# Kernel tuning notes

Measured on AMD Instinct MI355X. Metric: run time of the kernel, lower is better.

## Reference

```python
import jax, jax.numpy as jnp
import numpy as np

C = 1.0                      # curvature
PHI = 3.1415926 * 0.3        # Cosine phase (bias=False path)
ALPHA = 0.2                  # LeakyReLU negative slope
A_PARA = 0.5                 # a_para_GATLayer
EPS = 4e-3                   # float32 ball-projection epsilon (standard HGCN)
MIN_NORM = 1e-15
NEG_INF = -9e15              # matches -9000000000000000.0 in source


def project(x, c):
    # clamp points to lie inside the Poincare ball of curvature c
    norm = jnp.maximum(jnp.linalg.norm(x, axis=-1, keepdims=True), MIN_NORM)
    maxnorm = (1.0 - EPS) / jnp.sqrt(c)
    return jnp.where(norm > maxnorm, x / norm * maxnorm, x)


def artanh(x):
    return jnp.arctanh(jnp.clip(x, -1.0 + 1e-7, 1.0 - 1e-7))


def logmap0(p, c):
    # log map at the origin of the Poincare ball
    sqrt_c = c ** 0.5
    p_norm = jnp.maximum(jnp.linalg.norm(p, axis=-1, keepdims=True), MIN_NORM)
    return artanh(sqrt_c * p_norm) / (sqrt_c * p_norm) * p


def setup_inputs() -> dict:
    key = jax.random.key(0)
    k1, k2, k3, k4 = jax.random.split(key, 4)
    N, FIN, FOUT = 8192, 512, 128
    h = jax.random.normal(k1, (N, FIN), dtype=jnp.float32)
    adj = jax.random.randint(k2, (N, N), 0, 2, dtype=jnp.int32)
    # xavier_uniform with gain=1.414
    lim_w = 1.414 * np.sqrt(6.0 / (FIN + FOUT))
    W = jax.random.uniform(k3, (FIN, FOUT), jnp.float32, -lim_w, lim_w)
    lim_a = 1.414 * np.sqrt(6.0 / (2 * FOUT + 1))
    a = jax.random.uniform(k4, (2 * FOUT, 1), jnp.float32, -lim_a, lim_a)
    return {"h": h, "adj": adj, "W": W, "a": a}


def reference(h, adj, W, a):
    fout = W.shape[1]
    Wh = h @ W                                   # [N, F_out]
    Wh1 = Wh @ a[:fout]                          # [N, 1] source score
    Wh2 = Wh @ a[fout:]                          # [N, 1] target score
    e = jax.nn.leaky_relu(Wh1 + Wh2.T, ALPHA)    # [N, N]
    e = jnp.where(adj > 0, e, NEG_INF)
    attention = jax.nn.softmax(e, axis=1)        # dropout p=0 (eval): identity
    h_prime = attention @ Wh                     # [N, F_out]
    h_prime = logmap0(project(h_prime, C), C)
    # concat=True branch: ELU + a_para * A*cos(x + phi), A=1 (data_dim=-1)
    return jax.nn.elu(h_prime) + A_PARA * jnp.cos(h_prime + PHI)
```

## Files before the change

### kernel.cpp

```cpp
#include <hip/hip_runtime.h>
#include <hip/hip_bf16.h>
#include <math.h>

typedef short short8 __attribute__((ext_vector_type(8)));
typedef float f32x4 __attribute__((ext_vector_type(4)));

static constexpr int N = 8192;
static constexpr int FIN = 512;
static constexpr int FOUT = 128;
static constexpr float PHI = 3.1415926f * 0.3f;
static constexpr float A_PARA = 0.5f;
static constexpr float EPS_BALL = 4e-3f;
static constexpr float L2E = 1.4426950408889634f;

__device__ __forceinline__ unsigned short f2b(float f) {
    union { float f; unsigned u; } v; v.f = f;
    unsigned r = v.u + 0x7fffu + ((v.u >> 16) & 1u);
    return (unsigned short)(r >> 16);
}

__device__ __forceinline__ unsigned f2key(float x) {
    unsigned b = __float_as_uint(x);
    return (b & 0x80000000u) ? ~b : (b | 0x80000000u);
}
__device__ __forceinline__ float key2f(unsigned k) {
    unsigned b = (k & 0x80000000u) ? (k ^ 0x80000000u) : ~k;
    return __uint_as_float(b);
}

__device__ __forceinline__ short8 cvt8(float4 x0, float4 x1) {
    short8 r;
    r[0] = (short)f2b(x0.x); r[1] = (short)f2b(x0.y);
    r[2] = (short)f2b(x0.z); r[3] = (short)f2b(x0.w);
    r[4] = (short)f2b(x1.x); r[5] = (short)f2b(x1.y);
    r[6] = (short)f2b(x1.z); r[7] = (short)f2b(x1.w);
    return r;
}

__device__ __forceinline__ void cw(float* w, const int4 a, const float4 tv,
                                   float sA, float mA) {
    float z;
    z = sA + tv.x; w[0] = a.x > 0 ? __builtin_amdgcn_exp2f(fmaxf(z, 0.2f * z) - mA) : 0.f;
    z = sA + tv.y; w[1] = a.y > 0 ? __builtin_amdgcn_exp2f(fmaxf(z, 0.2f * z) - mA) : 0.f;
    z = sA + tv.z; w[2] = a.z > 0 ? __builtin_amdgcn_exp2f(fmaxf(z, 0.2f * z) - mA) : 0.f;
    z = sA + tv.w; w[3] = a.w > 0 ? __builtin_amdgcn_exp2f(fmaxf(z, 0.2f * z) - mA) : 0.f;
}

__global__ __launch_bounds__(256) void k0_wt(const float* __restrict__ W,
                                             unsigned short* __restrict__ Wt,
                                             unsigned* __restrict__ Tkey,
                                             float* __restrict__ denb) {
    __shared__ float sh[32][33];
    const int t = threadIdx.x;
    const int k0 = (blockIdx.x >> 2) * 32, c0 = (blockIdx.x & 3) * 32;
    {
        int r = t >> 3, c4 = (t & 7) * 4;
        float4 v = *(const float4*)(W + (size_t)(k0 + r) * FOUT + c0 + c4);
        sh[r][c4] = v.x; sh[r][c4 + 1] = v.y; sh[r][c4 + 2] = v.z; sh[r][c4 + 3] = v.w;
    }
    __syncthreads();
    int cc = t >> 3, k4 = (t & 7) * 4;
    ushort4 o;
    o.x = f2b(sh[k4][cc]); o.y = f2b(sh[k4 + 1][cc]);
    o.z = f2b(sh[k4 + 2][cc]); o.w = f2b(sh[k4 + 3][cc]);
    *(ushort4*)(Wt + (size_t)(c0 + cc) * FIN + k0 + k4) = o;
    if (blockIdx.x == 0) {
        if (t == 0) Tkey[0] = 0u;
        for (int i = t; i < N; i += 256) denb[i] = 0.f;
    }
}

__global__ __launch_bounds__(256) void k1_gemm(
    const float* __restrict__ h, const unsigned short* __restrict__ Wt,
    const float* __restrict__ a, unsigned short* __restrict__ whbt,
    float* __restrict__ s_out, float* __restrict__ t_out,
    unsigned* __restrict__ Tkey)
{
    __shared__ unsigned short hsb[2][32][72];
    __shared__ float sred[32][2], tred[32][2];
    const int t = threadIdx.x, lane = t & 63, wave = t >> 6;
    const int i0 = blockIdx.x * 32;
    const int wr = wave & 1, wc = wave >> 1;
    const int arow = lane & 15, g = lane >> 4;
    const int sr = t >> 3, sc = (t & 7) * 8;
    const float* hp = h + (size_t)(i0 + sr) * FIN + sc;

    float4 x0 = *(const float4*)hp, x1 = *(const float4*)(hp + 4);
    *(short8*)&hsb[0][sr][sc] = cvt8(x0, x1);
    __syncthreads();

    f32x4 acc[4];
    const f32x4 zz = {0.f, 0.f, 0.f, 0.f};
    #pragma unroll
    for (int cf = 0; cf < 4; ++cf) acc[cf] = zz;

    #pragma unroll 1
    for (int kt = 0; kt < 8; ++kt) {
        const int cur = kt & 1;
        float4 y0, y1;
        if (kt < 7) {
            y0 = *(const float4*)(hp + (kt + 1) * 64);
            y1 = *(const float4*)(hp + (kt + 1) * 64 + 4);
        }
        #pragma unroll
        for (int js = 0; js < 64; js += 32) {
            short8 af = *(const short8*)&hsb[cur][wr * 16 + arow][js + g * 8];
            #pragma unroll
            for (int cf = 0; cf < 4; ++cf) {
                const unsigned short* bp =
                    Wt + (size_t)(wc * 64 + cf * 16 + arow) * FIN + kt * 64 + js + g * 8;
                short8 bf = *(const short8*)bp;
                acc[cf] = __builtin_amdgcn_mfma_f32_16x16x32_bf16(af, bf, acc[cf], 0, 0, 0);
            }
        }
        if (kt < 7) {
            *(short8*)&hsb[cur ^ 1][sr][sc] = cvt8(y0, y1);
            __syncthreads();
        }
    }

    float a1v[4], a2v[4];
    #pragma unroll
    for (int cf = 0; cf < 4; ++cf) {
        int col = wc * 64 + cf * 16 + arow;
        a1v[cf] = a[col]; a2v[cf] = a[FOUT + col];
    }
    #pragma unroll
    for (int cf = 0; cf < 4; ++cf) {
        int col = wc * 64 + cf * 16 + arow;
        ushort4 o;
        o.x = f2b(acc[cf][0]); o.y = f2b(acc[cf][1]);
        o.z = f2b(acc[cf][2]); o.w = f2b(acc[cf][3]);
        *(ushort4*)(whbt + (size_t)col * N + i0 + wr * 16 + g * 4) = o;
    }
    #pragma unroll
    for (int q = 0; q < 4; ++q) {
        float sp = acc[0][q]*a1v[0] + acc[1][q]*a1v[1] + acc[2][q]*a1v[2] + acc[3][q]*a1v[3];
        float tp = acc[0][q]*a2v[0] + acc[1][q]*a2v[1] + acc[2][q]*a2v[2] + acc[3][q]*a2v[3];
        #pragma unroll
        for (int m = 1; m < 16; m <<= 1) {
            sp += __shfl_xor(sp, m, 16);
            tp += __shfl_xor(tp, m, 16);
        }
        if (arow == 0) {
            sred[wr * 16 + g * 4 + q][wc] = sp;
            tred[wr * 16 + g * 4 + q][wc] = tp;
        }
    }
    __syncthreads();
    if (t < 32) {
        float sp = (sred[t][0] + sred[t][1]) * L2E;
        float tp = (tred[t][0] + tred[t][1]) * L2E;
        s_out[i0 + t] = sp;
        t_out[i0 + t] = tp;
        float m = tp;
        #pragma unroll
        for (int d = 1; d < 32; d <<= 1) m = fmaxf(m, __shfl_xor(m, d, 32));
        if (t == 0) atomicMax(Tkey, f2key(m));
    }
}

__global__ __launch_bounds__(512, 4) void k3_attn(
    const int* __restrict__ adj, const unsigned short* __restrict__ whbt,
    const float* __restrict__ s_in, const float* __restrict__ t_in,
    const unsigned* __restrict__ Tkey,
    unsigned short* __restrict__ num_bf, float* __restrict__ num_f32,
    float* __restrict__ den_out, int slice_mode)
{
    __shared__ unsigned short bt[2][128][72];
    __shared__ float tl[1024];
    const int t = threadIdx.x, lane = t & 63, wave = t >> 6;
    const int jc = blockIdx.x & 7, it = blockIdx.x >> 3;
    const int i0 = it * 128, jbase = jc * 1024;

    tl[t] = t_in[jbase + t];
    tl[t + 512] = t_in[jbase + t + 512];

    const int arow = lane & 15, g = lane >> 4;
    const int grow = i0 + wave * 16 + arow;
    const float sA = s_in[grow];
    const float Tv = key2f(Tkey[0]);
    const float zT = sA + Tv;
    const float mA = fmaxf(zT, 0.2f * zT);
    const int* adjrow = adj + (size_t)grow * N;
    const int srow = t >> 2, scol = (t & 3) * 16;
    const unsigned short* sbase = whbt + (size_t)srow * N + jbase + scol;

    f32x4 acc[8];
    const f32x4 zz = {0.f, 0.f, 0.f, 0.f};
    #pragma unroll
    for (int c = 0; c < 8; ++c) acc[c] = zz;
    float den = 0.f;

    short8 sr0 = *(const short8*)sbase;
    short8 sr1 = *(const short8*)(sbase + 8);
    int4 av0 = *(const int4*)(adjrow + jbase + g * 8);
    int4 av1 = *(const int4*)(adjrow + jbase + g * 8 + 4);
    int4 av2 = *(const int4*)(adjrow + jbase + 32 + g * 8);
    int4 av3 = *(const int4*)(adjrow + jbase + 32 + g * 8 + 4);
    *(short8*)&bt[0][srow][scol]     = sr0;
    *(short8*)&bt[0][srow][scol + 8] = sr1;
    __syncthreads();

    #pragma unroll 1
    for (int jt = 0; jt < 16; ++jt) {
        const int cur = jt & 1, jl = jt * 64;
        short8 n0, n1;
        if (jt < 15) {
            const unsigned short* p = sbase + (jt + 1) * 64;
            n0 = *(const short8*)p;
            n1 = *(const short8*)(p + 8);
        }
        int4 an0, an1, an2, an3;
        if (jt < 15) {
            const int* ap = adjrow + jbase + jl + 64;
            an0 = *(const int4*)(ap + g * 8);
            an1 = *(const int4*)(ap + g * 8 + 4);
            an2 = *(const int4*)(ap + 32 + g * 8);
            an3 = *(const int4*)(ap + 32 + g * 8 + 4);
        }
        float4 ta = *(const float4*)&tl[jl + g * 8];
        float4 tb = *(const float4*)&tl[jl + g * 8 + 4];
        float4 tc = *(const float4*)&tl[jl + 32 + g * 8];
        float4 td = *(const float4*)&tl[jl + 32 + g * 8 + 4];
        float w[16];
        cw(&w[0],  av0, ta, sA, mA);
        cw(&w[4],  av1, tb, sA, mA);
        cw(&w[8],  av2, tc, sA, mA);
        cw(&w[12], av3, td, sA, mA);
        #pragma unroll
        for (int e = 0; e < 16; ++e) den += w[e];
        short8 af0, af1;
        #pragma unroll
        for (int e = 0; e < 8; ++e) {
            af0[e] = (short)f2b(w[e]);
            af1[e] = (short)f2b(w[8 + e]);
        }
        #pragma unroll
        for (int c = 0; c < 8; ++c) {
            short8 bf = *(const short8*)&bt[cur][c * 16 + arow][g * 8];
            acc[c] = __builtin_amdgcn_mfma_f32_16x16x32_bf16(af0, bf, acc[c], 0, 0, 0);
        }
        #pragma unroll
        for (int c = 0; c < 8; ++c) {
            short8 bf = *(const short8*)&bt[cur][c * 16 + arow][32 + g * 8];
            acc[c] = __builtin_amdgcn_mfma_f32_16x16x32_bf16(af1, bf, acc[c], 0, 0, 0);
        }
        if (jt < 15) {
            *(short8*)&bt[cur ^ 1][srow][scol]     = n0;
            *(short8*)&bt[cur ^ 1][srow][scol + 8] = n1;
            av0 = an0; av1 = an1; av2 = an2; av3 = an3;
            __syncthreads();
        }
    }

    den += __shfl_xor(den, 16, 64);
    den += __shfl_xor(den, 32, 64);
    if (g == 0) atomicAdd(&den_out[grow], den);

    const int orow0 = i0 + wave * 16;
    if (slice_mode) {
        unsigned short* dst = num_bf + (size_t)jc * ((size_t)N * FOUT);
        #pragma unroll
        for (int c = 0; c < 8; ++c)
            #pragma unroll
            for (int q = 0; q < 4; ++q)
                dst[(size_t)(orow0 + g * 4 + q) * FOUT + c * 16 + arow] = f2b(acc[c][q]);
    } else {
        #pragma unroll
        for (int c = 0; c < 8; ++c)
            #pragma unroll
            for (int q = 0; q < 4; ++q)
                atomicAdd(&num_f32[(size_t)(orow0 + g * 4 + q) * FOUT + c * 16 + arow], acc[c][q]);
    }
}

__global__ __launch_bounds__(256) void k4_epi(
    const unsigned short* __restrict__ numb, const float* __restrict__ numf,
    const float* __restrict__ den, float* __restrict__ out, int bfmode)
{
    const int row = blockIdx.x * 16 + (threadIdx.x >> 4);
    const int col0 = (threadIdx.x & 15) * 8;
    const float inv = 1.0f / den[row];
    float v[8] = {};
    if (bfmode) {
        #pragma unroll 1
        for (int s5 = 0; s5 < 8; ++s5) {
            short8 b = *(const short8*)(numb + (size_t)s5 * N * FOUT + (size_t)row * FOUT + col0);
            #pragma unroll
            for (int c = 0; c < 8; ++c)
                v[c] += __uint_as_float(((unsigned)(unsigned short)b[c]) << 16);
        }
    } else {
        #pragma unroll
        for (int c = 0; c < 8; ++c) v[c] = numf[(size_t)row * FOUT + col0 + c];
    }
    float ss = 0.f;
    #pragma unroll
    for (int c = 0; c < 8; ++c) { v[c] *= inv; ss += v[c] * v[c]; }
    #pragma unroll
    for (int m = 1; m < 16; m <<= 1) ss += __shfl_xor(ss, m, 16);
    float nrm = sqrtf(ss);
    const float maxn = 1.0f - EPS_BALL;
    float scale1 = nrm > maxn ? maxn / nrm : 1.0f;
    float pn = fminf(nrm, maxn);
    float fac;
    if (pn < 1e-6f) fac = scale1;
    else fac = scale1 * (0.5f * __logf((1.f + pn) / (1.f - pn))) / pn;
    float o[8];
    #pragma unroll
    for (int c = 0; c < 8; ++c) {
        float hv = v[c] * fac;
        float eluv = hv > 0.f ? hv : __expf(hv) - 1.f;
        o[c] = eluv + A_PARA * __cosf(hv + PHI);
    }
    float* op = out + (size_t)row * FOUT + col0;
    *(float4*)op = make_float4(o[0], o[1], o[2], o[3]);
    *(float4*)(op + 4) = make_float4(o[4], o[5], o[6], o[7]);
}

extern "C" void kernel_launch(void* const* d_in, const int* in_sizes, int n_in,
                              void* d_out, int out_size, void* d_ws, size_t ws_size,
                              hipStream_t stream) {
    const float* h   = (const float*)d_in[0];
    const int*   adj = (const int*)d_in[1];
    const float* W   = (const float*)d_in[2];
    const float* a   = (const float*)d_in[3];
    float* out = (float*)d_out;

    char* ws = (char*)d_ws;
    unsigned short* whbt = (unsigned short*)ws;
    size_t off = (size_t)N * FOUT * 2;
    unsigned short* Wt = (unsigned short*)(ws + off); off += (size_t)FOUT * FIN * 2;
    float* s  = (float*)(ws + off); off += (size_t)N * 4;
    float* tt = (float*)(ws + off); off += (size_t)N * 4;
    unsigned* Tkey = (unsigned*)(ws + off); off += 256;
    float* denb = (float*)(ws + off); off += (size_t)N * 4;
    const size_t slice_bytes = (size_t)N * FOUT * 2;
    const bool fast = ws_size >= off + 8 * slice_bytes;
    unsigned short* numb = fast ? (unsigned short*)(ws + off) : nullptr;

    if (!fast) hipMemsetAsync(out, 0, (size_t)N * FOUT * 4, stream);

    k0_wt<<<64, 256, 0, stream>>>(W, Wt, Tkey, denb);
    k1_gemm<<<N / 32, 256, 0, stream>>>(h, Wt, a, whbt, s, tt, Tkey);
    k3_attn<<<512, 512, 0, stream>>>(adj, whbt, s, tt, Tkey, numb, out, denb, fast ? 1 : 0);
    k4_epi<<<N / 16, 256, 0, stream>>>(numb, out, denb, out, fast ? 1 : 0);
}
```

Before: 97.20 us.

## Process two 16-row groups per wave in attention kernel to reuse B tiles

Each wave now handles 32 output rows (two 16-row MFMA groups), so every LDS B-fragment read feeds two MFMAs. The row tile per block doubles to 256, and the grid halves to 256 blocks with launch bounds relaxed to 2 blocks per CU. Weight conversion to bf16 uses the library intrinsic instead of the manual rounding. This aims to cut LDS traffic and per-tile overhead, at the cost of higher register pressure and fewer blocks (256 for a 256-CU device), which may hurt latency hiding.

After: 104.6 us. 7.6% more time.

```diff
diff --git a/kernel.cpp b/kernel.cpp
--- a/kernel.cpp
+++ b/kernel.cpp
@@ -17,6 +17,11 @@
     union { float f; unsigned u; } v; v.f = f;
     unsigned r = v.u + 0x7fffu + ((v.u >> 16) & 1u);
     return (unsigned short)(r >> 16);
+}
+
+__device__ __forceinline__ short f2bn(float f) {
+    __hip_bfloat16 h = __float2bfloat16(f);
+    return *reinterpret_cast<short*>(&h);
 }
 
 __device__ __forceinline__ unsigned f2key(float x) {
@@ -160,7 +165,7 @@
     }
 }
 
-__global__ __launch_bounds__(512, 4) void k3_attn(
+__global__ __launch_bounds__(512, 2) void k3_attn(
     const int* __restrict__ adj, const unsigned short* __restrict__ whbt,
     const float* __restrict__ s_in, const float* __restrict__ t_in,
     const unsigned* __restrict__ Tkey,
@@ -171,33 +176,41 @@
     __shared__ float tl[1024];
     const int t = threadIdx.x, lane = t & 63, wave = t >> 6;
     const int jc = blockIdx.x & 7, it = blockIdx.x >> 3;
-    const int i0 = it * 128, jbase = jc * 1024;
+    const int i0 = it * 256, jbase = jc * 1024;
 
     tl[t] = t_in[jbase + t];
     tl[t + 512] = t_in[jbase + t + 512];
 
     const int arow = lane & 15, g = lane >> 4;
-    const int grow = i0 + wave * 16 + arow;
-    const float sA = s_in[grow];
+    const int grow0 = i0 + wave * 32 + arow;
+    const int grow1 = grow0 + 16;
     const float Tv = key2f(Tkey[0]);
-    const float zT = sA + Tv;
-    const float mA = fmaxf(zT, 0.2f * zT);
-    const int* adjrow = adj + (size_t)grow * N;
+    const float sA0 = s_in[grow0];
+    const float sA1 = s_in[grow1];
+    const float z0 = sA0 + Tv, z1 = sA1 + Tv;
+    const float mA0 = fmaxf(z0, 0.2f * z0);
+    const float mA1 = fmaxf(z1, 0.2f * z1);
+    const int* ar0 = adj + (size_t)grow0 * N;
+    const int* ar1 = adj + (size_t)grow1 * N;
     const int srow = t >> 2, scol = (t & 3) * 16;
     const unsigned short* sbase = whbt + (size_t)srow * N + jbase + scol;
 
-    f32x4 acc[8];
+    f32x4 acc0[8], acc1[8];
     const f32x4 zz = {0.f, 0.f, 0.f, 0.f};
     #pragma unroll
-    for (int c = 0; c < 8; ++c) acc[c] = zz;
-    float den = 0.f;
+    for (int c = 0; c < 8; ++c) { acc0[c] = zz; acc1[c] = zz; }
+    float den0 = 0.f, den1 = 0.f;
 
     short8 sr0 = *(const short8*)sbase;
     short8 sr1 = *(const short8*)(sbase + 8);
-    int4 av0 = *(const int4*)(adjrow + jbase + g * 8);
-    int4 av1 = *(const int4*)(adjrow + jbase + g * 8 + 4);
-    int4 av2 = *(const int4*)(adjrow + jbase + 32 + g * 8);
-    int4 av3 = *(const int4*)(adjrow + jbase + 32 + g * 8 + 4);
+    int4 p00 = *(const int4*)(ar0 + jbase + g * 8);
+    int4 p01 = *(const int4*)(ar0 + jbase + g * 8 + 4);
+    int4 p02 = *(const int4*)(ar0 + jbase + 32 + g * 8);
+    int4 p03 = *(const int4*)(ar0 + jbase + 32 + g * 8 + 4);
+    int4 p10 = *(const int4*)(ar1 + jbase + g * 8);
+    int4 p11 = *(const int4*)(ar1 + jbase + g * 8 + 4);
+    int4 p12 = *(const int4*)(ar1 + jbase + 32 + g * 8);
+    int4 p13 = *(const int4*)(ar1 + jbase + 32 + g * 8 + 4);
     *(short8*)&bt[0][srow][scol]     = sr0;
     *(short8*)&bt[0][srow][scol + 8] = sr1;
     __syncthreads();
@@ -211,67 +224,90 @@
             n0 = *(const short8*)p;
             n1 = *(const short8*)(p + 8);
         }
-        int4 an0, an1, an2, an3;
+        int4 q00, q01, q02, q03, q10, q11, q12, q13;
         if (jt < 15) {
-            const int* ap = adjrow + jbase + jl + 64;
-            an0 = *(const int4*)(ap + g * 8);
-            an1 = *(const int4*)(ap + g * 8 + 4);
-            an2 = *(const int4*)(ap + 32 + g * 8);
-            an3 = *(const int4*)(ap + 32 + g * 8 + 4);
+            const int* a0 = ar0 + jbase + jl + 64;
+            const int* a1 = ar1 + jbase + jl + 64;
+            q00 = *(const int4*)(a0 + g * 8);
+            q01 = *(const int4*)(a0 + g * 8 + 4);
+            q02 = *(const int4*)(a0 + 32 + g * 8);
+            q03 = *(const int4*)(a0 + 32 + g * 8 + 4);
+            q10 = *(const int4*)(a1 + g * 8);
+            q11 = *(const int4*)(a1 + g * 8 + 4);
+            q12 = *(const int4*)(a1 + 32 + g * 8);
+            q13 = *(const int4*)(a1 + 32 + g * 8 + 4);
         }
         float4 ta = *(const float4*)&tl[jl + g * 8];
         float4 tb = *(const float4*)&tl[jl + g * 8 + 4];
         float4 tc = *(const float4*)&tl[jl + 32 + g * 8];
         float4 td = *(const float4*)&tl[jl + 32 + g * 8 + 4];
-        float w[16];
-        cw(&w[0],  av0, ta, sA, mA);
-        cw(&w[4],  av1, tb, sA, mA);
-        cw(&w[8],  av2, tc, sA, mA);
-        cw(&w[12], av3, td, sA, mA);
-        #pragma unroll
-        for (int e = 0; e < 16; ++e) den += w[e];
-        short8 af0, af1;
+        float w0[16], w1[16];
+        cw(&w0[0],  p00, ta, sA0, mA0);
+        cw(&w0[4],  p01, tb, sA0, mA0);
+        cw(&w0[8],  p02, tc, sA0, mA0);
+        cw(&w0[12], p03, td, sA0, mA0);
+        cw(&w1[0],  p10, ta, sA1, mA1);
+        cw(&w1[4],  p11, tb, sA1, mA1);
+        cw(&w1[8],  p12, tc, sA1, mA1);
+        cw(&w1[12], p13, td, sA1, mA1);
+        #pragma unroll
+        for (int e = 0; e < 16; ++e) { den0 += w0[e]; den1 += w1[e]; }
+        short8 a00, a01, a10, a11;
         #pragma unroll
         for (int e = 0; e < 8; ++e) {
-            af0[e] = (short)f2b(w[e]);
-            af1[e] = (short)f2b(w[8 + e]);
+            a00[e] = f2bn(w0[e]);
+            a01[e] = f2bn(w0[8 + e]);
+            a10[e] = f2bn(w1[e]);
+            a11[e] = f2bn(w1[8 + e]);
         }
         #pragma unroll
         for (int c = 0; c < 8; ++c) {
             short8 bf = *(const short8*)&bt[cur][c * 16 + arow][g * 8];
-            acc[c] = __builtin_amdgcn_mfma_f32_16x16x32_bf16(af0, bf, acc[c], 0, 0, 0);
+            acc0[c] = __builtin_amdgcn_mfma_f32_16x16x32_bf16(a00, bf, acc0[c], 0, 0, 0);
+            acc1[c] = __builtin_amdgcn_mfma_f32_16x16x32_bf16(a10, bf, acc1[c], 0, 0, 0);
         }
         #pragma unroll
         for (int c = 0; c < 8; ++c) {
             short8 bf = *(const short8*)&bt[cur][c * 16 + arow][32 + g * 8];
-            acc[c] = __builtin_amdgcn_mfma_f32_16x16x32_bf16(af1, bf, acc[c], 0, 0, 0);
+            acc0[c] = __builtin_amdgcn_mfma_f32_16x16x32_bf16(a01, bf, acc0[c], 0, 0, 0);
+            acc1[c] = __builtin_amdgcn_mfma_f32_16x16x32_bf16(a11, bf, acc1[c], 0, 0, 0);
         }
         if (jt < 15) {
             *(short8*)&bt[cur ^ 1][srow][scol]     = n0;
             *(short8*)&bt[cur ^ 1][srow][scol + 8] = n1;
-            av0 = an0; av1 = an1; av2 = an2; av3 = an3;
+            p00 = q00; p01 = q01; p02 = q02; p03 = q03;
+            p10 = q10; p11 = q11; p12 = q12; p13 = q13;
             __syncthreads();
         }
     }
 
-    den += __shfl_xor(den, 16, 64);
-    den += __shfl_xor(den, 32, 64);
-    if (g == 0) atomicAdd(&den_out[grow], den);
-
-    const int orow0 = i0 + wave * 16;
+    den0 += __shfl_xor(den0, 16, 64);
+    den0 += __shfl_xor(den0, 32, 64);
+    den1 += __shfl_xor(den1, 16, 64);
+    den1 += __shfl_xor(den1, 32, 64);
+    if (g == 0) {
+        atomicAdd(&den_out[grow0], den0);
+        atomicAdd(&den_out[grow1], den1);
+    }
+
+    const int orow0 = i0 + wave * 32;
     if (slice_mode) {
         unsigned short* dst = num_bf + (size_t)jc * ((size_t)N * FOUT);
         #pragma unroll
         for (int c = 0; c < 8; ++c)
             #pragma unroll
-            for (int q = 0; q < 4; ++q)
-                dst[(size_t)(orow0 + g * 4 + q) * FOUT + c * 16 + arow] = f2b(acc[c][q]);
+            for (int q = 0; q < 4; ++q) {
+                dst[(size_t)(orow0 + g * 4 + q) * FOUT + c * 16 + arow] = f2b(acc0[c][q]);
+                dst[(size_t)(orow0 + 16 + g * 4 + q) * FOUT + c * 16 + arow] = f2b(acc1[c][q]);
+            }
     } else {
         #pragma unroll
         for (int c = 0; c < 8; ++c)
             #pragma unroll
-            for (int q = 0; q < 4; ++q)
-                atomicAdd(&num_f32[(size_t)(orow0 + g * 4 + q) * FOUT + c * 16 + arow], acc[c][q]);
+            for (int q = 0; q < 4; ++q) {
+                atomicAdd(&num_f32[(size_t)(orow0 + g * 4 + q) * FOUT + c * 16 + arow], acc0[c][q]);
+                atomicAdd(&num_f32[(size_t)(orow0 + 16 + g * 4 + q) * FOUT + c * 16 + arow], acc1[c][q]);
+            }
     }
 }
 
@@ -344,6 +380,6 @@
 
     k0_wt<<<64, 256, 0, stream>>>(W, Wt, Tkey, denb);
     k1_gemm<<<N / 32, 256, 0, stream>>>(h, Wt, a, whbt, s, tt, Tkey);
-    k3_attn<<<512, 512, 0, stream>>>(adj, whbt, s, tt, Tkey, numb, out, denb, fast ? 1 : 0);
+    k3_attn<<<256, 512, 0, stream>>>(adj, whbt, s, tt, Tkey, numb, out, denb, fast ? 1 : 0);
     k4_epi<<<N / 16, 256, 0, stream>>>(numb, out, denb, out, fast ? 1 : 0);
 }
```
